# Kernel optimization log

Measured on AMD Instinct MI355X. Metric: run time of the kernel, lower is better.

The kernel has to match this reference:

```python
import jax, jax.numpy as jnp
import numpy as np

D_MODEL = 256
EXPERT_DIM = 512
NUM_EXPERTS = 8
TOP_K = 2
SEQ_LEN = 2048
BATCH = 2


def setup_inputs() -> dict:
    key = jax.random.key(0)
    ks = jax.random.split(key, 8)
    s = 0.02
    x = jax.random.normal(ks[0], (SEQ_LEN, BATCH, D_MODEL), dtype=jnp.float32)
    # gate: torch Linear(d_model, num_experts); store as [d, E] so logits = x @ Wg + bg
    Wg = jax.random.normal(ks[1], (D_MODEL, NUM_EXPERTS), dtype=jnp.float32) * s
    bg = jax.random.normal(ks[2], (NUM_EXPERTS,), dtype=jnp.float32) * s
    bias = jnp.zeros((NUM_EXPERTS,), dtype=jnp.float32)  # dynamic routing bias
    # experts: Linear(d, h) -> ReLU -> Linear(h, d), stacked over E
    W1 = jax.random.normal(ks[3], (NUM_EXPERTS, D_MODEL, EXPERT_DIM), dtype=jnp.float32) * s
    b1 = jax.random.normal(ks[4], (NUM_EXPERTS, EXPERT_DIM), dtype=jnp.float32) * s
    W2 = jax.random.normal(ks[5], (NUM_EXPERTS, EXPERT_DIM, D_MODEL), dtype=jnp.float32) * s
    b2 = jax.random.normal(ks[6], (NUM_EXPERTS, D_MODEL), dtype=jnp.float32) * s
    return {"x": x, "Wg": Wg, "bg": bg, "bias": bias, "W1": W1, "b1": b1, "W2": W2, "b2": b2}


def reference(x, Wg, bg, bias, W1, b1, W2, b2):
    # x: [seq, batch, d] -> flatten tokens
    x_flat = x.reshape(-1, D_MODEL)                      # [T, d]
    gate_logits = x_flat @ Wg + bg + bias                # [T, E]
    topk_vals, topk_idx = jax.lax.top_k(gate_logits, TOP_K)   # [T, K]
    # torch code subtracts the row max (topk_vals[:, :1], sorted desc) then softmaxes;
    # jax.nn.softmax is the same stable computation.
    topk_w = jax.nn.softmax(topk_vals, axis=-1)          # [T, K]
    # combine weights over experts: zero for unchosen experts -> exact same math
    # as the masked gather + scatter-add in the original loop.
    combine = (jax.nn.one_hot(topk_idx, NUM_EXPERTS, dtype=x.dtype)
               * topk_w[..., None]).sum(axis=1)          # [T, E]
    h = jax.nn.relu(jnp.einsum('td,edh->teh', x_flat, W1) + b1)   # [T, E, H]
    y = jnp.einsum('teh,ehd->ted', h, W2) + b2                     # [T, E, d]
    out = jnp.einsum('ted,te->td', y, combine)                     # [T, d]
    # dropout is identity in eval mode (p applied only in training)
    return out.reshape(x.shape)
```

## Files before the change

### kernel.cpp

```cpp
#include <hip/hip_runtime.h>
#include <hip/hip_bf16.h>
#include <math.h>

#define D_MODEL 256
#define EXPERT_DIM 512
#define NUM_EXPERTS 8
#define T_TOKENS 4096
#define TM 32
#define XS_LD 264

typedef unsigned short ushort_t;
typedef short short8_t __attribute__((ext_vector_type(8)));
typedef float f32x4 __attribute__((ext_vector_type(4)));

__device__ __forceinline__ ushort_t f2bf(float f) {
    unsigned int u = __float_as_uint(f);
    u += 0x7FFFu + ((u >> 16) & 1u);
    return (ushort_t)(u >> 16);
}

__global__ __launch_bounds__(256) void convert_frag_kernel(
    const float* __restrict__ W1, const float* __restrict__ W2,
    ushort_t* __restrict__ W1f, ushort_t* __restrict__ W2f)
{
    int gid = blockIdx.x * 256 + threadIdx.x;
    bool isW2 = gid >= 131072;
    int idx = isW2 ? gid - 131072 : gid;
    int lane = idx & 63;
    int l15 = lane & 15, quad = lane >> 4;
    int ks = (idx >> 6) & 7;
    ushort_t o[8];
    if (!isW2) {
        int ntile = (idx >> 9) & 31, e = idx >> 14;
        int nn = ntile * 16 + l15;
        int k0 = ks * 32 + quad * 8;
        const float* s = W1 + ((size_t)e * D_MODEL + k0) * EXPERT_DIM + nn;
#pragma unroll
        for (int j = 0; j < 8; ++j) o[j] = f2bf(s[j * EXPERT_DIM]);
        *(int4*)(W1f + (size_t)idx * 8) = *(int4*)o;
    } else {
        int ntile = (idx >> 9) & 15, half = (idx >> 13) & 1, e = idx >> 14;
        int nn = ntile * 16 + l15;
        int k0 = half * 256 + ks * 32 + quad * 8;
        const float* s = W2 + ((size_t)e * EXPERT_DIM + k0) * D_MODEL + nn;
#pragma unroll
        for (int j = 0; j < 8; ++j) o[j] = f2bf(s[j * D_MODEL]);
        *(int4*)(W2f + (size_t)idx * 8) = *(int4*)o;
    }
}

__global__ __launch_bounds__(256) void moe_gate_kernel(
    const float* __restrict__ x, const float* __restrict__ Wg,
    const float* __restrict__ bg, const float* __restrict__ bias,
    int* __restrict__ counts, int* __restrict__ lists, float* __restrict__ wts)
{
    __shared__ int lcount[NUM_EXPERTS];
    __shared__ int lbase[NUM_EXPERTS];
    const int tid = threadIdx.x;
    const int t = blockIdx.x * 256 + tid;
    if (tid < NUM_EXPERTS) lcount[tid] = 0;

    const float4* x4 = reinterpret_cast<const float4*>(x + t * D_MODEL);
    float acc[NUM_EXPERTS];
#pragma unroll
    for (int e = 0; e < NUM_EXPERTS; ++e) acc[e] = 0.f;
    for (int i4 = 0; i4 < D_MODEL / 4; ++i4) {
        float4 xv = x4[i4];
        const float* wrow = Wg + i4 * 4 * NUM_EXPERTS;
#pragma unroll
        for (int e = 0; e < NUM_EXPERTS; ++e) {
            acc[e] += xv.x * wrow[e]
                    + xv.y * wrow[NUM_EXPERTS + e]
                    + xv.z * wrow[2 * NUM_EXPERTS + e]
                    + xv.w * wrow[3 * NUM_EXPERTS + e];
        }
    }
    float v0 = -3.0e38f, v1 = -3.0e38f; int i0 = 0, i1 = 0;
#pragma unroll
    for (int e = 0; e < NUM_EXPERTS; ++e) {
        float v = acc[e] + bg[e] + bias[e];
        if (v > v0) { v1 = v0; i1 = i0; v0 = v; i0 = e; }
        else if (v > v1) { v1 = v; i1 = e; }
    }
    float e1 = __expf(v1 - v0);
    float inv = 1.f / (1.f + e1);
    float w0 = inv, w1 = e1 * inv;

    __syncthreads();
    int p0 = atomicAdd(&lcount[i0], 1);
    int p1 = atomicAdd(&lcount[i1], 1);
    __syncthreads();
    if (tid < NUM_EXPERTS) lbase[tid] = atomicAdd(&counts[tid], lcount[tid]);
    __syncthreads();
    int q0 = lbase[i0] + p0;
    int q1 = lbase[i1] + p1;
    lists[i0 * T_TOKENS + q0] = t;  wts[i0 * T_TOKENS + q0] = w0;
    lists[i1 * T_TOKENS + q1] = t;  wts[i1 * T_TOKENS + q1] = w1;
}

__global__ __launch_bounds__(256) void moe_expert_mfma(
    const float* __restrict__ x,
    const ushort_t* __restrict__ W1f, const float* __restrict__ b1,
    const ushort_t* __restrict__ W2f, const float* __restrict__ b2,
    const int* __restrict__ counts, const int* __restrict__ lists,
    const float* __restrict__ wts, float* __restrict__ out)
{
    const int e = blockIdx.x;
    const int half = blockIdx.y;
    const int n = counts[e];
    const int base = blockIdx.z * TM;
    if (base >= n) return;
    const int m = min(TM, n - base);

    __shared__ ushort_t Xs[TM * XS_LD];
    __shared__ ushort_t Hs[TM * XS_LD];
    __shared__ int   toks[TM];
    __shared__ float wt_s[TM];

    const int tid = threadIdx.x;
    if (tid < TM) {
        const int* lst = lists + e * T_TOKENS + base;
        const float* wr = wts + e * T_TOKENS + base;
        toks[tid] = (tid < m) ? lst[tid] : -1;
        wt_s[tid] = (tid < m) ? wr[tid] : 0.f;
    }
    __syncthreads();

    for (int c = tid; c < TM * 32; c += 256) {
        int r = c >> 5, c8 = c & 31;
        int tk = toks[r];
        ushort_t o[8];
        if (tk >= 0) {
            const float* src = x + tk * D_MODEL + c8 * 8;
            float4 v0 = *(const float4*)src;
            float4 v1 = *(const float4*)(src + 4);
            o[0] = f2bf(v0.x); o[1] = f2bf(v0.y); o[2] = f2bf(v0.z); o[3] = f2bf(v0.w);
            o[4] = f2bf(v1.x); o[5] = f2bf(v1.y); o[6] = f2bf(v1.z); o[7] = f2bf(v1.w);
        } else {
#pragma unroll
            for (int j = 0; j < 8; ++j) o[j] = 0;
        }
        *(int4*)(Xs + r * XS_LD + c8 * 8) = *(int4*)o;
    }
    __syncthreads();

    const int lane = tid & 63;
    const int w = tid >> 6;
    const int l15 = lane & 15;
    const int quad = lane >> 4;

    const ushort_t* W1p = W1f + (size_t)(e * 32 + half * 16 + w * 4) * 4096 + lane * 8;
    float b1v[4];
#pragma unroll
    for (int nt = 0; nt < 4; ++nt)
        b1v[nt] = b1[e * EXPERT_DIM + half * 256 + w * 64 + nt * 16 + l15];

    f32x4 acc1[2][4] = {};
    short8_t bc[4];
#pragma unroll
    for (int nt = 0; nt < 4; ++nt) bc[nt] = *(const short8_t*)(W1p + nt * 4096);

    for (int ks = 0; ks < 8; ++ks) {
        short8_t bn[4];
        if (ks < 7) {
#pragma unroll
            for (int nt = 0; nt < 4; ++nt)
                bn[nt] = *(const short8_t*)(W1p + nt * 4096 + (ks + 1) * 512);
        }
        short8_t a0 = *(const short8_t*)(Xs + l15 * XS_LD + ks * 32 + quad * 8);
        short8_t a1 = *(const short8_t*)(Xs + (16 + l15) * XS_LD + ks * 32 + quad * 8);
#pragma unroll
        for (int nt = 0; nt < 4; ++nt) {
            acc1[0][nt] = __builtin_amdgcn_mfma_f32_16x16x32_bf16(a0, bc[nt], acc1[0][nt], 0, 0, 0);
            acc1[1][nt] = __builtin_amdgcn_mfma_f32_16x16x32_bf16(a1, bc[nt], acc1[1][nt], 0, 0, 0);
        }
        if (ks < 7) {
#pragma unroll
            for (int nt = 0; nt < 4; ++nt) bc[nt] = bn[nt];
        }
    }
#pragma unroll
    for (int mt = 0; mt < 2; ++mt)
#pragma unroll
        for (int nt = 0; nt < 4; ++nt)
#pragma unroll
            for (int r = 0; r < 4; ++r) {
                int row = mt * 16 + quad * 4 + r;
                int col = w * 64 + nt * 16 + l15;
                float h = fmaxf(acc1[mt][nt][r] + b1v[nt], 0.f);
                Hs[row * XS_LD + col] = f2bf(h);
            }
    __syncthreads();

    const ushort_t* W2p = W2f + (size_t)((e * 2 + half) * 16 + w * 4) * 4096 + lane * 8;
    float b2v[4];
#pragma unroll
    for (int nt = 0; nt < 4; ++nt)
        b2v[nt] = half ? b2[e * D_MODEL + w * 64 + nt * 16 + l15] : 0.f;

    f32x4 acc2[2][4] = {};
    short8_t bc2[4];
#pragma unroll
    for (int nt = 0; nt < 4; ++nt) bc2[nt] = *(const short8_t*)(W2p + nt * 4096);

    for (int ks = 0; ks < 8; ++ks) {
        short8_t bn2[4];
        if (ks < 7) {
#pragma unroll
            for (int nt = 0; nt < 4; ++nt)
                bn2[nt] = *(const short8_t*)(W2p + nt * 4096 + (ks + 1) * 512);
        }
        short8_t a0 = *(const short8_t*)(Hs + l15 * XS_LD + ks * 32 + quad * 8);
        short8_t a1 = *(const short8_t*)(Hs + (16 + l15) * XS_LD + ks * 32 + quad * 8);
#pragma unroll
        for (int nt = 0; nt < 4; ++nt) {
            acc2[0][nt] = __builtin_amdgcn_mfma_f32_16x16x32_bf16(a0, bc2[nt], acc2[0][nt], 0, 0, 0);
            acc2[1][nt] = __builtin_amdgcn_mfma_f32_16x16x32_bf16(a1, bc2[nt], acc2[1][nt], 0, 0, 0);
        }
        if (ks < 7) {
#pragma unroll
            for (int nt = 0; nt < 4; ++nt) bc2[nt] = bn2[nt];
        }
    }

#pragma unroll
    for (int mt = 0; mt < 2; ++mt)
#pragma unroll
        for (int nt = 0; nt < 4; ++nt)
#pragma unroll
            for (int r = 0; r < 4; ++r) {
                int row = mt * 16 + quad * 4 + r;
                int tk = toks[row];
                if (tk >= 0) {
                    int col = w * 64 + nt * 16 + l15;
                    atomicAdd(&out[tk * D_MODEL + col],
                              wt_s[row] * (acc2[mt][nt][r] + b2v[nt]));
                }
            }
}

extern "C" void kernel_launch(void* const* d_in, const int* in_sizes, int n_in,
                              void* d_out, int out_size, void* d_ws, size_t ws_size,
                              hipStream_t stream)
{
    const float* x    = (const float*)d_in[0];
    const float* Wg   = (const float*)d_in[1];
    const float* bg   = (const float*)d_in[2];
    const float* bias = (const float*)d_in[3];
    const float* W1   = (const float*)d_in[4];
    const float* b1   = (const float*)d_in[5];
    const float* W2   = (const float*)d_in[6];
    const float* b2   = (const float*)d_in[7];
    float* out = (float*)d_out;

    char* ws = (char*)d_ws;
    int*      counts = (int*)ws;
    int*      lists  = (int*)(ws + 256);
    float*    wts    = (float*)(ws + 256 + 131072);
    ushort_t* W1f    = (ushort_t*)(ws + 256 + 262144);
    ushort_t* W2f    = (ushort_t*)(ws + 256 + 262144 + 2097152);

    hipMemsetAsync(out, 0, (size_t)out_size * sizeof(float), stream);
    hipMemsetAsync(counts, 0, NUM_EXPERTS * sizeof(int), stream);

    convert_frag_kernel<<<1024, 256, 0, stream>>>(W1, W2, W1f, W2f);

    moe_gate_kernel<<<T_TOKENS / 256, 256, 0, stream>>>(
        x, Wg, bg, bias, counts, lists, wts);

    moe_expert_mfma<<<dim3(NUM_EXPERTS, 2, T_TOKENS / TM), 256, 0, stream>>>(
        x, W1f, b1, W2f, b2, counts, lists, wts, out);
}
```

Before: 120.4 us.

## Split expert hidden dim into quarters, fuse gate with weight conversion, replace memsets

```diff
diff --git a/kernel.cpp b/kernel.cpp
--- a/kernel.cpp
+++ b/kernel.cpp
@@ -8,6 +8,7 @@
 #define T_TOKENS 4096
 #define TM 32
 #define XS_LD 264
+#define HS_LD 136
 
 typedef unsigned short ushort_t;
 typedef short short8_t __attribute__((ext_vector_type(8)));
@@ -19,83 +20,101 @@
     return (ushort_t)(u >> 16);
 }
 
-__global__ __launch_bounds__(256) void convert_frag_kernel(
-    const float* __restrict__ W1, const float* __restrict__ W2,
-    ushort_t* __restrict__ W1f, ushort_t* __restrict__ W2f)
-{
-    int gid = blockIdx.x * 256 + threadIdx.x;
-    bool isW2 = gid >= 131072;
-    int idx = isW2 ? gid - 131072 : gid;
-    int lane = idx & 63;
-    int l15 = lane & 15, quad = lane >> 4;
-    int ks = (idx >> 6) & 7;
-    ushort_t o[8];
-    if (!isW2) {
-        int ntile = (idx >> 9) & 31, e = idx >> 14;
-        int nn = ntile * 16 + l15;
-        int k0 = ks * 32 + quad * 8;
-        const float* s = W1 + ((size_t)e * D_MODEL + k0) * EXPERT_DIM + nn;
-#pragma unroll
-        for (int j = 0; j < 8; ++j) o[j] = f2bf(s[j * EXPERT_DIM]);
-        *(int4*)(W1f + (size_t)idx * 8) = *(int4*)o;
-    } else {
-        int ntile = (idx >> 9) & 15, half = (idx >> 13) & 1, e = idx >> 14;
-        int nn = ntile * 16 + l15;
-        int k0 = half * 256 + ks * 32 + quad * 8;
-        const float* s = W2 + ((size_t)e * EXPERT_DIM + k0) * D_MODEL + nn;
-#pragma unroll
-        for (int j = 0; j < 8; ++j) o[j] = f2bf(s[j * D_MODEL]);
-        *(int4*)(W2f + (size_t)idx * 8) = *(int4*)o;
-    }
-}
-
-__global__ __launch_bounds__(256) void moe_gate_kernel(
+__global__ __launch_bounds__(256) void zero_kernel(float* __restrict__ out,
+                                                   int* __restrict__ counts)
+{
+    int i = blockIdx.x * 256 + threadIdx.x;
+    *(float4*)(out + (size_t)i * 4) = make_float4(0.f, 0.f, 0.f, 0.f);
+    if (i < NUM_EXPERTS) counts[i] = 0;
+}
+
+__global__ __launch_bounds__(256) void prep_kernel(
     const float* __restrict__ x, const float* __restrict__ Wg,
     const float* __restrict__ bg, const float* __restrict__ bias,
+    const float* __restrict__ W1, const float* __restrict__ W2,
+    ushort_t* __restrict__ W1f, ushort_t* __restrict__ W2f,
     int* __restrict__ counts, int* __restrict__ lists, float* __restrict__ wts)
 {
+    __shared__ float xs[256][33];
     __shared__ int lcount[NUM_EXPERTS];
     __shared__ int lbase[NUM_EXPERTS];
+
     const int tid = threadIdx.x;
-    const int t = blockIdx.x * 256 + tid;
-    if (tid < NUM_EXPERTS) lcount[tid] = 0;
-
-    const float4* x4 = reinterpret_cast<const float4*>(x + t * D_MODEL);
-    float acc[NUM_EXPERTS];
-#pragma unroll
-    for (int e = 0; e < NUM_EXPERTS; ++e) acc[e] = 0.f;
-    for (int i4 = 0; i4 < D_MODEL / 4; ++i4) {
-        float4 xv = x4[i4];
-        const float* wrow = Wg + i4 * 4 * NUM_EXPERTS;
+    if (blockIdx.x < 16) {
+        const int tbase = blockIdx.x * 256;
+        if (tid < NUM_EXPERTS) lcount[tid] = 0;
+        float acc[NUM_EXPERTS];
+#pragma unroll
+        for (int e = 0; e < NUM_EXPERTS; ++e) acc[e] = 0.f;
+
+        for (int kc = 0; kc < 8; ++kc) {
+            __syncthreads();
+#pragma unroll
+            for (int it = 0; it < 8; ++it) {
+                int pos = it * 256 + tid;
+                int tl = pos >> 3, c4 = pos & 7;
+                float4 v = *(const float4*)(x + (size_t)(tbase + tl) * D_MODEL
+                                            + kc * 32 + c4 * 4);
+                xs[tl][c4 * 4 + 0] = v.x; xs[tl][c4 * 4 + 1] = v.y;
+                xs[tl][c4 * 4 + 2] = v.z; xs[tl][c4 * 4 + 3] = v.w;
+            }
+            __syncthreads();
+            for (int k = 0; k < 32; ++k) {
+                float xv = xs[tid][k];
+                const float* wr = Wg + (kc * 32 + k) * NUM_EXPERTS;
+#pragma unroll
+                for (int e = 0; e < NUM_EXPERTS; ++e) acc[e] += xv * wr[e];
+            }
+        }
+        float v0 = -3.0e38f, v1 = -3.0e38f; int i0 = 0, i1 = 0;
 #pragma unroll
         for (int e = 0; e < NUM_EXPERTS; ++e) {
-            acc[e] += xv.x * wrow[e]
-                    + xv.y * wrow[NUM_EXPERTS + e]
-                    + xv.z * wrow[2 * NUM_EXPERTS + e]
-                    + xv.w * wrow[3 * NUM_EXPERTS + e];
-        }
-    }
-    float v0 = -3.0e38f, v1 = -3.0e38f; int i0 = 0, i1 = 0;
-#pragma unroll
-    for (int e = 0; e < NUM_EXPERTS; ++e) {
-        float v = acc[e] + bg[e] + bias[e];
-        if (v > v0) { v1 = v0; i1 = i0; v0 = v; i0 = e; }
-        else if (v > v1) { v1 = v; i1 = e; }
-    }
-    float e1 = __expf(v1 - v0);
-    float inv = 1.f / (1.f + e1);
-    float w0 = inv, w1 = e1 * inv;
-
-    __syncthreads();
-    int p0 = atomicAdd(&lcount[i0], 1);
-    int p1 = atomicAdd(&lcount[i1], 1);
-    __syncthreads();
-    if (tid < NUM_EXPERTS) lbase[tid] = atomicAdd(&counts[tid], lcount[tid]);
-    __syncthreads();
-    int q0 = lbase[i0] + p0;
-    int q1 = lbase[i1] + p1;
-    lists[i0 * T_TOKENS + q0] = t;  wts[i0 * T_TOKENS + q0] = w0;
-    lists[i1 * T_TOKENS + q1] = t;  wts[i1 * T_TOKENS + q1] = w1;
+            float v = acc[e] + bg[e] + bias[e];
+            if (v > v0) { v1 = v0; i1 = i0; v0 = v; i0 = e; }
+            else if (v > v1) { v1 = v; i1 = e; }
+        }
+        float e1 = __expf(v1 - v0);
+        float inv = 1.f / (1.f + e1);
+        float w0 = inv, w1 = e1 * inv;
+
+        int p0 = atomicAdd(&lcount[i0], 1);
+        int p1 = atomicAdd(&lcount[i1], 1);
+        __syncthreads();
+        if (tid < NUM_EXPERTS) lbase[tid] = atomicAdd(&counts[tid], lcount[tid]);
+        __syncthreads();
+        int t = tbase + tid;
+        int q0 = lbase[i0] + p0;
+        int q1 = lbase[i1] + p1;
+        lists[i0 * T_TOKENS + q0] = t;  wts[i0 * T_TOKENS + q0] = w0;
+        lists[i1 * T_TOKENS + q1] = t;  wts[i1 * T_TOKENS + q1] = w1;
+    } else {
+        int gid = (blockIdx.x - 16) * 256 + tid;
+        bool isW2 = gid >= 131072;
+        int idx = isW2 ? gid - 131072 : gid;
+        int lane = idx & 63;
+        int l15 = lane & 15, quad = lane >> 4;
+        ushort_t o[8];
+        if (!isW2) {
+            int ks = (idx >> 6) & 7;
+            int ntile = (idx >> 9) & 31, e = idx >> 14;
+            int nn = ntile * 16 + l15;
+            int k0 = ks * 32 + quad * 8;
+            const float* s = W1 + ((size_t)e * D_MODEL + k0) * EXPERT_DIM + nn;
+#pragma unroll
+            for (int j = 0; j < 8; ++j) o[j] = f2bf(s[j * EXPERT_DIM]);
+            *(int4*)(W1f + (size_t)idx * 8) = *(int4*)o;
+        } else {
+            int ks = (idx >> 6) & 3;
+            int ntile = (idx >> 8) & 15;
+            int q = (idx >> 12) & 3, e = idx >> 14;
+            int nn = ntile * 16 + l15;
+            int k0 = q * 128 + ks * 32 + quad * 8;
+            const float* s = W2 + ((size_t)e * EXPERT_DIM + k0) * D_MODEL + nn;
+#pragma unroll
+            for (int j = 0; j < 8; ++j) o[j] = f2bf(s[j * D_MODEL]);
+            *(int4*)(W2f + (size_t)idx * 8) = *(int4*)o;
+        }
+    }
 }
 
 __global__ __launch_bounds__(256) void moe_expert_mfma(
@@ -106,18 +125,28 @@
     const float* __restrict__ wts, float* __restrict__ out)
 {
     const int e = blockIdx.x;
-    const int half = blockIdx.y;
+    const int q = blockIdx.y;
     const int n = counts[e];
     const int base = blockIdx.z * TM;
     if (base >= n) return;
     const int m = min(TM, n - base);
 
     __shared__ ushort_t Xs[TM * XS_LD];
-    __shared__ ushort_t Hs[TM * XS_LD];
+    __shared__ ushort_t Hs[TM * HS_LD];
     __shared__ int   toks[TM];
     __shared__ float wt_s[TM];
 
     const int tid = threadIdx.x;
+    const int lane = tid & 63;
+    const int w = tid >> 6;
+    const int l15 = lane & 15;
+    const int quad = lane >> 4;
+
+    const ushort_t* W1p = W1f + (size_t)(e * 32 + q * 8 + w * 2) * 4096 + lane * 8;
+    short8_t bc[2];
+    bc[0] = *(const short8_t*)(W1p);
+    bc[1] = *(const short8_t*)(W1p + 4096);
+
     if (tid < TM) {
         const int* lst = lists + e * T_TOKENS + base;
         const float* wr = wts + e * T_TOKENS + base;
@@ -131,7 +160,7 @@
         int tk = toks[r];
         ushort_t o[8];
         if (tk >= 0) {
-            const float* src = x + tk * D_MODEL + c8 * 8;
+            const float* src = x + (size_t)tk * D_MODEL + c8 * 8;
             float4 v0 = *(const float4*)src;
             float4 v1 = *(const float4*)(src + 4);
             o[0] = f2bf(v0.x); o[1] = f2bf(v0.y); o[2] = f2bf(v0.z); o[3] = f2bf(v0.w);
@@ -144,80 +173,66 @@
     }
     __syncthreads();
 
-    const int lane = tid & 63;
-    const int w = tid >> 6;
-    const int l15 = lane & 15;
-    const int quad = lane >> 4;
-
-    const ushort_t* W1p = W1f + (size_t)(e * 32 + half * 16 + w * 4) * 4096 + lane * 8;
-    float b1v[4];
-#pragma unroll
-    for (int nt = 0; nt < 4; ++nt)
-        b1v[nt] = b1[e * EXPERT_DIM + half * 256 + w * 64 + nt * 16 + l15];
-
-    f32x4 acc1[2][4] = {};
-    short8_t bc[4];
-#pragma unroll
-    for (int nt = 0; nt < 4; ++nt) bc[nt] = *(const short8_t*)(W1p + nt * 4096);
-
+    float b1v[2];
+#pragma unroll
+    for (int nt = 0; nt < 2; ++nt)
+        b1v[nt] = b1[e * EXPERT_DIM + (q * 8 + w * 2 + nt) * 16 + l15];
+
+    f32x4 acc1[2][2] = {};
     for (int ks = 0; ks < 8; ++ks) {
-        short8_t bn[4];
+        short8_t bn[2];
         if (ks < 7) {
-#pragma unroll
-            for (int nt = 0; nt < 4; ++nt)
-                bn[nt] = *(const short8_t*)(W1p + nt * 4096 + (ks + 1) * 512);
+            bn[0] = *(const short8_t*)(W1p + (ks + 1) * 512);
+            bn[1] = *(const short8_t*)(W1p + 4096 + (ks + 1) * 512);
         }
         short8_t a0 = *(const short8_t*)(Xs + l15 * XS_LD + ks * 32 + quad * 8);
         short8_t a1 = *(const short8_t*)(Xs + (16 + l15) * XS_LD + ks * 32 + quad * 8);
 #pragma unroll
-        for (int nt = 0; nt < 4; ++nt) {
+        for (int nt = 0; nt < 2; ++nt) {
             acc1[0][nt] = __builtin_amdgcn_mfma_f32_16x16x32_bf16(a0, bc[nt], acc1[0][nt], 0, 0, 0);
             acc1[1][nt] = __builtin_amdgcn_mfma_f32_16x16x32_bf16(a1, bc[nt], acc1[1][nt], 0, 0, 0);
         }
-        if (ks < 7) {
-#pragma unroll
-            for (int nt = 0; nt < 4; ++nt) bc[nt] = bn[nt];
-        }
-    }
+        if (ks < 7) { bc[0] = bn[0]; bc[1] = bn[1]; }
+    }
+
+    const ushort_t* W2p = W2f + (size_t)((e * 4 + q) * 16 + w * 4) * 2048 + lane * 8;
+    short8_t bc2[4];
+#pragma unroll
+    for (int nt = 0; nt < 4; ++nt) bc2[nt] = *(const short8_t*)(W2p + nt * 2048);
+    float b2v[4];
+#pragma unroll
+    for (int nt = 0; nt < 4; ++nt)
+        b2v[nt] = (q == 0) ? b2[e * D_MODEL + w * 64 + nt * 16 + l15] : 0.f;
+
 #pragma unroll
     for (int mt = 0; mt < 2; ++mt)
 #pragma unroll
-        for (int nt = 0; nt < 4; ++nt)
+        for (int nt = 0; nt < 2; ++nt)
 #pragma unroll
             for (int r = 0; r < 4; ++r) {
                 int row = mt * 16 + quad * 4 + r;
-                int col = w * 64 + nt * 16 + l15;
+                int col = w * 32 + nt * 16 + l15;
                 float h = fmaxf(acc1[mt][nt][r] + b1v[nt], 0.f);
-                Hs[row * XS_LD + col] = f2bf(h);
+                Hs[row * HS_LD + col] = f2bf(h);
             }
     __syncthreads();
 
-    const ushort_t* W2p = W2f + (size_t)((e * 2 + half) * 16 + w * 4) * 4096 + lane * 8;
-    float b2v[4];
-#pragma unroll
-    for (int nt = 0; nt < 4; ++nt)
-        b2v[nt] = half ? b2[e * D_MODEL + w * 64 + nt * 16 + l15] : 0.f;
-
     f32x4 acc2[2][4] = {};
-    short8_t bc2[4];
-#pragma unroll
-    for (int nt = 0; nt < 4; ++nt) bc2[nt] = *(const short8_t*)(W2p + nt * 4096);
-
-    for (int ks = 0; ks < 8; ++ks) {
+    for (int ks = 0; ks < 4; ++ks) {
         short8_t bn2[4];
-        if (ks < 7) {
+        if (ks < 3) {
 #pragma unroll
             for (int nt = 0; nt < 4; ++nt)
-                bn2[nt] = *(const short8_t*)(W2p + nt * 4096 + (ks + 1) * 512);
-        }
-        short8_t a0 = *(const short8_t*)(Hs + l15 * XS_LD + ks * 32 + quad * 8);
-        short8_t a1 = *(const short8_t*)(Hs + (16 + l15) * XS_LD + ks * 32 + quad * 8);
+                bn2[nt] = *(const short8_t*)(W2p + nt * 2048 + (ks + 1) * 512);
+        }
+        short8_t a0 = *(const short8_t*)(Hs + l15 * HS_LD + ks * 32 + quad * 8);
+        short8_t a1 = *(const short8_t*)(Hs + (16 + l15) * HS_LD + ks * 32 + quad * 8);
 #pragma unroll
         for (int nt = 0; nt < 4; ++nt) {
             acc2[0][nt] = __builtin_amdgcn_mfma_f32_16x16x32_bf16(a0, bc2[nt], acc2[0][nt], 0, 0, 0);
             acc2[1][nt] = __builtin_amdgcn_mfma_f32_16x16x32_bf16(a1, bc2[nt], acc2[1][nt], 0, 0, 0);
         }
-        if (ks < 7) {
+        if (ks < 3) {
 #pragma unroll
             for (int nt = 0; nt < 4; ++nt) bc2[nt] = bn2[nt];
         }
@@ -233,7 +248,7 @@
                 int tk = toks[row];
                 if (tk >= 0) {
                     int col = w * 64 + nt * 16 + l15;
-                    atomicAdd(&out[tk * D_MODEL + col],
+                    atomicAdd(&out[(size_t)tk * D_MODEL + col],
                               wt_s[row] * (acc2[mt][nt][r] + b2v[nt]));
                 }
             }
@@ -260,14 +275,11 @@
     ushort_t* W1f    = (ushort_t*)(ws + 256 + 262144);
     ushort_t* W2f    = (ushort_t*)(ws + 256 + 262144 + 2097152);
 
-    hipMemsetAsync(out, 0, (size_t)out_size * sizeof(float), stream);
-    hipMemsetAsync(counts, 0, NUM_EXPERTS * sizeof(int), stream);
-
-    convert_frag_kernel<<<1024, 256, 0, stream>>>(W1, W2, W1f, W2f);
-
-    moe_gate_kernel<<<T_TOKENS / 256, 256, 0, stream>>>(
-        x, Wg, bg, bias, counts, lists, wts);
-
-    moe_expert_mfma<<<dim3(NUM_EXPERTS, 2, T_TOKENS / TM), 256, 0, stream>>>(
+    zero_kernel<<<1024, 256, 0, stream>>>(out, counts);
+
+    prep_kernel<<<1040, 256, 0, stream>>>(
+        x, Wg, bg, bias, W1, W2, W1f, W2f, counts, lists, wts);
+
+    moe_expert_mfma<<<dim3(NUM_EXPERTS, 4, T_TOKENS / TM), 256, 0, stream>>>(
         x, W1f, b1, W2f, b2, counts, lists, wts, out);
 }
```

Result: slower. 133.9 us (+11.2%).

## Merge gate and weight conversion, replace atomic scatter with buffered combine pass

Applied to the files above, without the earlier changes.

```diff
diff --git a/kernel.cpp b/kernel.cpp
--- a/kernel.cpp
+++ b/kernel.cpp
@@ -19,83 +19,99 @@
     return (ushort_t)(u >> 16);
 }
 
-__global__ __launch_bounds__(256) void convert_frag_kernel(
-    const float* __restrict__ W1, const float* __restrict__ W2,
-    ushort_t* __restrict__ W1f, ushort_t* __restrict__ W2f)
-{
-    int gid = blockIdx.x * 256 + threadIdx.x;
-    bool isW2 = gid >= 131072;
-    int idx = isW2 ? gid - 131072 : gid;
-    int lane = idx & 63;
-    int l15 = lane & 15, quad = lane >> 4;
-    int ks = (idx >> 6) & 7;
-    ushort_t o[8];
-    if (!isW2) {
-        int ntile = (idx >> 9) & 31, e = idx >> 14;
-        int nn = ntile * 16 + l15;
-        int k0 = ks * 32 + quad * 8;
-        const float* s = W1 + ((size_t)e * D_MODEL + k0) * EXPERT_DIM + nn;
-#pragma unroll
-        for (int j = 0; j < 8; ++j) o[j] = f2bf(s[j * EXPERT_DIM]);
-        *(int4*)(W1f + (size_t)idx * 8) = *(int4*)o;
-    } else {
-        int ntile = (idx >> 9) & 15, half = (idx >> 13) & 1, e = idx >> 14;
-        int nn = ntile * 16 + l15;
-        int k0 = half * 256 + ks * 32 + quad * 8;
-        const float* s = W2 + ((size_t)e * EXPERT_DIM + k0) * D_MODEL + nn;
-#pragma unroll
-        for (int j = 0; j < 8; ++j) o[j] = f2bf(s[j * D_MODEL]);
-        *(int4*)(W2f + (size_t)idx * 8) = *(int4*)o;
-    }
-}
-
-__global__ __launch_bounds__(256) void moe_gate_kernel(
+__global__ void zero_counts_kernel(int* __restrict__ counts)
+{
+    if (threadIdx.x < NUM_EXPERTS) counts[threadIdx.x] = 0;
+}
+
+__global__ __launch_bounds__(256) void prep_kernel(
     const float* __restrict__ x, const float* __restrict__ Wg,
     const float* __restrict__ bg, const float* __restrict__ bias,
-    int* __restrict__ counts, int* __restrict__ lists, float* __restrict__ wts)
-{
+    const float* __restrict__ W1, const float* __restrict__ W2,
+    ushort_t* __restrict__ W1f, ushort_t* __restrict__ W2f,
+    int* __restrict__ counts, int* __restrict__ lists,
+    float* __restrict__ wts, int* __restrict__ slots)
+{
+    __shared__ float xs[256][33];
     __shared__ int lcount[NUM_EXPERTS];
     __shared__ int lbase[NUM_EXPERTS];
+
     const int tid = threadIdx.x;
-    const int t = blockIdx.x * 256 + tid;
-    if (tid < NUM_EXPERTS) lcount[tid] = 0;
-
-    const float4* x4 = reinterpret_cast<const float4*>(x + t * D_MODEL);
-    float acc[NUM_EXPERTS];
-#pragma unroll
-    for (int e = 0; e < NUM_EXPERTS; ++e) acc[e] = 0.f;
-    for (int i4 = 0; i4 < D_MODEL / 4; ++i4) {
-        float4 xv = x4[i4];
-        const float* wrow = Wg + i4 * 4 * NUM_EXPERTS;
+    if (blockIdx.x < 16) {
+        const int tbase = blockIdx.x * 256;
+        if (tid < NUM_EXPERTS) lcount[tid] = 0;
+        float acc[NUM_EXPERTS];
+#pragma unroll
+        for (int e = 0; e < NUM_EXPERTS; ++e) acc[e] = 0.f;
+
+        for (int kc = 0; kc < 8; ++kc) {
+            __syncthreads();
+#pragma unroll
+            for (int it = 0; it < 8; ++it) {
+                int pos = it * 256 + tid;
+                int tl = pos >> 3, c4 = pos & 7;
+                float4 v = *(const float4*)(x + (size_t)(tbase + tl) * D_MODEL
+                                            + kc * 32 + c4 * 4);
+                xs[tl][c4 * 4 + 0] = v.x; xs[tl][c4 * 4 + 1] = v.y;
+                xs[tl][c4 * 4 + 2] = v.z; xs[tl][c4 * 4 + 3] = v.w;
+            }
+            __syncthreads();
+            for (int k = 0; k < 32; ++k) {
+                float xv = xs[tid][k];
+                const float* wr = Wg + (kc * 32 + k) * NUM_EXPERTS;
+#pragma unroll
+                for (int e = 0; e < NUM_EXPERTS; ++e) acc[e] += xv * wr[e];
+            }
+        }
+        float v0 = -3.0e38f, v1 = -3.0e38f; int i0 = 0, i1 = 0;
 #pragma unroll
         for (int e = 0; e < NUM_EXPERTS; ++e) {
-            acc[e] += xv.x * wrow[e]
-                    + xv.y * wrow[NUM_EXPERTS + e]
-                    + xv.z * wrow[2 * NUM_EXPERTS + e]
-                    + xv.w * wrow[3 * NUM_EXPERTS + e];
-        }
-    }
-    float v0 = -3.0e38f, v1 = -3.0e38f; int i0 = 0, i1 = 0;
-#pragma unroll
-    for (int e = 0; e < NUM_EXPERTS; ++e) {
-        float v = acc[e] + bg[e] + bias[e];
-        if (v > v0) { v1 = v0; i1 = i0; v0 = v; i0 = e; }
-        else if (v > v1) { v1 = v; i1 = e; }
-    }
-    float e1 = __expf(v1 - v0);
-    float inv = 1.f / (1.f + e1);
-    float w0 = inv, w1 = e1 * inv;
-
-    __syncthreads();
-    int p0 = atomicAdd(&lcount[i0], 1);
-    int p1 = atomicAdd(&lcount[i1], 1);
-    __syncthreads();
-    if (tid < NUM_EXPERTS) lbase[tid] = atomicAdd(&counts[tid], lcount[tid]);
-    __syncthreads();
-    int q0 = lbase[i0] + p0;
-    int q1 = lbase[i1] + p1;
-    lists[i0 * T_TOKENS + q0] = t;  wts[i0 * T_TOKENS + q0] = w0;
-    lists[i1 * T_TOKENS + q1] = t;  wts[i1 * T_TOKENS + q1] = w1;
+            float v = acc[e] + bg[e] + bias[e];
+            if (v > v0) { v1 = v0; i1 = i0; v0 = v; i0 = e; }
+            else if (v > v1) { v1 = v; i1 = e; }
+        }
+        float e1 = __expf(v1 - v0);
+        float inv = 1.f / (1.f + e1);
+        float w0 = inv, w1 = e1 * inv;
+
+        int p0 = atomicAdd(&lcount[i0], 1);
+        int p1 = atomicAdd(&lcount[i1], 1);
+        __syncthreads();
+        if (tid < NUM_EXPERTS) lbase[tid] = atomicAdd(&counts[tid], lcount[tid]);
+        __syncthreads();
+        int t = tbase + tid;
+        int q0 = lbase[i0] + p0;
+        int q1 = lbase[i1] + p1;
+        lists[i0 * T_TOKENS + q0] = t;  wts[i0 * T_TOKENS + q0] = w0;
+        lists[i1 * T_TOKENS + q1] = t;  wts[i1 * T_TOKENS + q1] = w1;
+        slots[t * 2 + 0] = i0 * T_TOKENS + q0;
+        slots[t * 2 + 1] = i1 * T_TOKENS + q1;
+    } else {
+        int gid = (blockIdx.x - 16) * 256 + tid;
+        bool isW2 = gid >= 131072;
+        int idx = isW2 ? gid - 131072 : gid;
+        int lane = idx & 63;
+        int l15 = lane & 15, quad = lane >> 4;
+        int ks = (idx >> 6) & 7;
+        ushort_t o[8];
+        if (!isW2) {
+            int ntile = (idx >> 9) & 31, e = idx >> 14;
+            int nn = ntile * 16 + l15;
+            int k0 = ks * 32 + quad * 8;
+            const float* s = W1 + ((size_t)e * D_MODEL + k0) * EXPERT_DIM + nn;
+#pragma unroll
+            for (int j = 0; j < 8; ++j) o[j] = f2bf(s[j * EXPERT_DIM]);
+            *(int4*)(W1f + (size_t)idx * 8) = *(int4*)o;
+        } else {
+            int ntile = (idx >> 9) & 15, half = (idx >> 13) & 1, e = idx >> 14;
+            int nn = ntile * 16 + l15;
+            int k0 = half * 256 + ks * 32 + quad * 8;
+            const float* s = W2 + ((size_t)e * EXPERT_DIM + k0) * D_MODEL + nn;
+#pragma unroll
+            for (int j = 0; j < 8; ++j) o[j] = f2bf(s[j * D_MODEL]);
+            *(int4*)(W2f + (size_t)idx * 8) = *(int4*)o;
+        }
+    }
 }
 
 __global__ __launch_bounds__(256) void moe_expert_mfma(
@@ -103,7 +119,7 @@
     const ushort_t* __restrict__ W1f, const float* __restrict__ b1,
     const ushort_t* __restrict__ W2f, const float* __restrict__ b2,
     const int* __restrict__ counts, const int* __restrict__ lists,
-    const float* __restrict__ wts, float* __restrict__ out)
+    const float* __restrict__ wts, float* __restrict__ ybuf)
 {
     const int e = blockIdx.x;
     const int half = blockIdx.y;
@@ -118,6 +134,16 @@
     __shared__ float wt_s[TM];
 
     const int tid = threadIdx.x;
+    const int lane = tid & 63;
+    const int w = tid >> 6;
+    const int l15 = lane & 15;
+    const int quad = lane >> 4;
+
+    const ushort_t* W1p = W1f + (size_t)(e * 32 + half * 16 + w * 4) * 4096 + lane * 8;
+    short8_t bc[4];
+#pragma unroll
+    for (int nt = 0; nt < 4; ++nt) bc[nt] = *(const short8_t*)(W1p + nt * 4096);
+
     if (tid < TM) {
         const int* lst = lists + e * T_TOKENS + base;
         const float* wr = wts + e * T_TOKENS + base;
@@ -131,7 +157,7 @@
         int tk = toks[r];
         ushort_t o[8];
         if (tk >= 0) {
-            const float* src = x + tk * D_MODEL + c8 * 8;
+            const float* src = x + (size_t)tk * D_MODEL + c8 * 8;
             float4 v0 = *(const float4*)src;
             float4 v1 = *(const float4*)(src + 4);
             o[0] = f2bf(v0.x); o[1] = f2bf(v0.y); o[2] = f2bf(v0.z); o[3] = f2bf(v0.w);
@@ -144,22 +170,12 @@
     }
     __syncthreads();
 
-    const int lane = tid & 63;
-    const int w = tid >> 6;
-    const int l15 = lane & 15;
-    const int quad = lane >> 4;
-
-    const ushort_t* W1p = W1f + (size_t)(e * 32 + half * 16 + w * 4) * 4096 + lane * 8;
     float b1v[4];
 #pragma unroll
     for (int nt = 0; nt < 4; ++nt)
         b1v[nt] = b1[e * EXPERT_DIM + half * 256 + w * 64 + nt * 16 + l15];
 
     f32x4 acc1[2][4] = {};
-    short8_t bc[4];
-#pragma unroll
-    for (int nt = 0; nt < 4; ++nt) bc[nt] = *(const short8_t*)(W1p + nt * 4096);
-
     for (int ks = 0; ks < 8; ++ks) {
         short8_t bn[4];
         if (ks < 7) {
@@ -179,6 +195,16 @@
             for (int nt = 0; nt < 4; ++nt) bc[nt] = bn[nt];
         }
     }
+
+    const ushort_t* W2p = W2f + (size_t)((e * 2 + half) * 16 + w * 4) * 4096 + lane * 8;
+    short8_t bc2[4];
+#pragma unroll
+    for (int nt = 0; nt < 4; ++nt) bc2[nt] = *(const short8_t*)(W2p + nt * 4096);
+    float b2v[4];
+#pragma unroll
+    for (int nt = 0; nt < 4; ++nt)
+        b2v[nt] = half ? b2[e * D_MODEL + w * 64 + nt * 16 + l15] : 0.f;
+
 #pragma unroll
     for (int mt = 0; mt < 2; ++mt)
 #pragma unroll
@@ -192,17 +218,7 @@
             }
     __syncthreads();
 
-    const ushort_t* W2p = W2f + (size_t)((e * 2 + half) * 16 + w * 4) * 4096 + lane * 8;
-    float b2v[4];
-#pragma unroll
-    for (int nt = 0; nt < 4; ++nt)
-        b2v[nt] = half ? b2[e * D_MODEL + w * 64 + nt * 16 + l15] : 0.f;
-
     f32x4 acc2[2][4] = {};
-    short8_t bc2[4];
-#pragma unroll
-    for (int nt = 0; nt < 4; ++nt) bc2[nt] = *(const short8_t*)(W2p + nt * 4096);
-
     for (int ks = 0; ks < 8; ++ks) {
         short8_t bn2[4];
         if (ks < 7) {
@@ -223,6 +239,7 @@
         }
     }
 
+    float* yrow = ybuf + ((size_t)(half * NUM_EXPERTS + e) * T_TOKENS + base) * D_MODEL;
 #pragma unroll
     for (int mt = 0; mt < 2; ++mt)
 #pragma unroll
@@ -230,13 +247,33 @@
 #pragma unroll
             for (int r = 0; r < 4; ++r) {
                 int row = mt * 16 + quad * 4 + r;
-                int tk = toks[row];
-                if (tk >= 0) {
+                if (row < m) {
                     int col = w * 64 + nt * 16 + l15;
-                    atomicAdd(&out[tk * D_MODEL + col],
-                              wt_s[row] * (acc2[mt][nt][r] + b2v[nt]));
+                    yrow[(size_t)row * D_MODEL + col] =
+                        wt_s[row] * (acc2[mt][nt][r] + b2v[nt]);
                 }
             }
+}
+
+__global__ __launch_bounds__(256) void combine_kernel(
+    const int* __restrict__ slots, const float* __restrict__ ybuf,
+    float* __restrict__ out)
+{
+    int gid = blockIdx.x * 256 + threadIdx.x;
+    int t = gid >> 6, lane = gid & 63;
+    int s0 = slots[t * 2 + 0];
+    int s1 = slots[t * 2 + 1];
+    const size_t H = (size_t)NUM_EXPERTS * T_TOKENS * D_MODEL;
+    float4 a = ((const float4*)(ybuf + (size_t)s0 * D_MODEL))[lane];
+    float4 b = ((const float4*)(ybuf + (size_t)s0 * D_MODEL + H))[lane];
+    float4 c = ((const float4*)(ybuf + (size_t)s1 * D_MODEL))[lane];
+    float4 d = ((const float4*)(ybuf + (size_t)s1 * D_MODEL + H))[lane];
+    float4 r;
+    r.x = a.x + b.x + c.x + d.x;
+    r.y = a.y + b.y + c.y + d.y;
+    r.z = a.z + b.z + c.z + d.z;
+    r.w = a.w + b.w + c.w + d.w;
+    ((float4*)(out + (size_t)t * D_MODEL))[lane] = r;
 }
 
 extern "C" void kernel_launch(void* const* d_in, const int* in_sizes, int n_in,
@@ -257,17 +294,18 @@
     int*      counts = (int*)ws;
     int*      lists  = (int*)(ws + 256);
     float*    wts    = (float*)(ws + 256 + 131072);
-    ushort_t* W1f    = (ushort_t*)(ws + 256 + 262144);
-    ushort_t* W2f    = (ushort_t*)(ws + 256 + 262144 + 2097152);
-
-    hipMemsetAsync(out, 0, (size_t)out_size * sizeof(float), stream);
-    hipMemsetAsync(counts, 0, NUM_EXPERTS * sizeof(int), stream);
-
-    convert_frag_kernel<<<1024, 256, 0, stream>>>(W1, W2, W1f, W2f);
-
-    moe_gate_kernel<<<T_TOKENS / 256, 256, 0, stream>>>(
-        x, Wg, bg, bias, counts, lists, wts);
+    int*      slots  = (int*)(ws + 256 + 262144);
+    ushort_t* W1f    = (ushort_t*)(ws + 256 + 294912);
+    ushort_t* W2f    = (ushort_t*)(ws + 256 + 294912 + 2097152);
+    float*    ybuf   = (float*)(ws + 256 + 294912 + 4194304);
+
+    zero_counts_kernel<<<1, 64, 0, stream>>>(counts);
+
+    prep_kernel<<<1040, 256, 0, stream>>>(
+        x, Wg, bg, bias, W1, W2, W1f, W2f, counts, lists, wts, slots);
 
     moe_expert_mfma<<<dim3(NUM_EXPERTS, 2, T_TOKENS / TM), 256, 0, stream>>>(
-        x, W1f, b1, W2f, b2, counts, lists, wts, out);
-}
+        x, W1f, b1, W2f, b2, counts, lists, wts, ybuf);
+
+    combine_kernel<<<T_TOKENS * 64 / 256, 256, 0, stream>>>(slots, ybuf, out);
+}
```

Result: faster. 117.2 us (-2.7%).
